# Optimization experiments

Measured on AMD Instinct MI355X. Metric: run time of the kernel, lower is better.

## Reference

```python
import jax, jax.numpy as jnp
import numpy as np

HEADS = 8
DIM_HEAD = 64
INNER = HEADS * DIM_HEAD  # 512
EPS = 1e-6


def layer_norm(x, gamma, beta):
    mu = jnp.mean(x, axis=-1, keepdims=True)
    var = jnp.var(x, axis=-1, keepdims=True)
    return (x - mu) * jax.lax.rsqrt(var + EPS) * gamma + beta


def setup_inputs() -> dict:
    key = jax.random.key(0)
    ks = jax.random.split(key, 8)
    b, n = 2, 2048
    s = lambda d: 1.0 / np.sqrt(d)
    return {
        "x": jax.random.normal(ks[0], (b, n, INNER), dtype=jnp.float32),
        # weights stored input-major: y = x @ W
        "w_qkv": jax.random.normal(ks[1], (INNER, 3 * INNER), dtype=jnp.float32) * s(INNER),
        "w_out": jax.random.normal(ks[2], (INNER, INNER), dtype=jnp.float32) * s(INNER),
        "b_out": jax.random.normal(ks[3], (INNER,), dtype=jnp.float32) * 0.01,
        "w_ff1": jax.random.normal(ks[4], (INNER, 4 * INNER), dtype=jnp.float32) * s(INNER),
        "w_ff2": jax.random.normal(ks[5], (4 * INNER, INNER), dtype=jnp.float32) * s(4 * INNER),
        "g1": jnp.ones((INNER,), dtype=jnp.float32),
        "be1": jnp.zeros((INNER,), dtype=jnp.float32),
        "g2": jnp.ones((INNER,), dtype=jnp.float32),
        "be2": jnp.zeros((INNER,), dtype=jnp.float32),
    }


def reference(x, w_qkv, w_out, b_out, w_ff1, w_ff2, g1, be1, g2, be2):
    b, n, _ = x.shape
    scale = DIM_HEAD ** (-0.5)
    qkv = x @ w_qkv  # [b, n, 3*inner]
    qkv = qkv.reshape(b, n, 3, HEADS, DIM_HEAD)
    q = qkv[:, :, 0].transpose(0, 2, 1, 3)  # [b, h, n, d]
    k = qkv[:, :, 1].transpose(0, 2, 1, 3)
    v = qkv[:, :, 2].transpose(0, 2, 1, 3)
    dots = jnp.einsum('bhqd,bhkd->bhqk', q, k) * scale
    attn = jax.nn.softmax(dots, axis=-1)
    out = jnp.einsum('bhqk,bhkd->bhqd', attn, v)
    out = out.transpose(0, 2, 1, 3).reshape(b, n, INNER)
    out = out @ w_out + b_out
    attn_res = layer_norm(x + out, g1, be1)
    # NOTE: no activation between the two FFN linears (faithful to source)
    ff = (attn_res @ w_ff1) @ w_ff2
    return layer_norm(attn_res + ff, g2, be2)
```

## Files before the change

kernel.cpp:

```cpp
#include <hip/hip_runtime.h>
#include <hip/hip_bf16.h>
#include <cstdint>
#include <cstddef>
#include <math.h>

#define HEADS 8
#define DHEAD 64
#define INNER 512
#define BATCH 2
#define SEQ   2048
#define MROWS (BATCH*SEQ)
#define LN_EPS 1e-6f
#define KSPLIT 4
#define KCHUNK (SEQ/KSPLIT)
#define QSCALE 0.18033688011110918f

typedef unsigned short u16;
typedef __attribute__((ext_vector_type(8))) short short8;
typedef __attribute__((ext_vector_type(4))) short short4v;
typedef __attribute__((ext_vector_type(4))) float f32x4;

#define MFMA16(a,b,c) __builtin_amdgcn_mfma_f32_16x16x32_bf16((a),(b),(c),0,0,0)
#if __has_builtin(__builtin_amdgcn_mfma_f32_16x16x16bf16_1k)
#define HAVE_MFMA16K16 1
#define MFMA16K16(a,b,c) __builtin_amdgcn_mfma_f32_16x16x16bf16_1k((a),(b),(c),0,0,0)
#endif

__device__ __forceinline__ float bf2f(u16 u) {
    union { float f; uint32_t i; } x; x.i = ((uint32_t)u) << 16; return x.f;
}
__device__ __forceinline__ u16 f2bf(float f) {
    __hip_bfloat16 h = __float2bfloat16(f);
    return *reinterpret_cast<u16*>(&h);
}
__device__ __forceinline__ void gl_lds16(const void* g, void* l) {
    __builtin_amdgcn_global_load_lds(
        (const __attribute__((address_space(1))) void*)g,
        (__attribute__((address_space(3))) void*)l, 16, 0, 0);
}

__global__ void prep_kernel(const float* __restrict__ x, u16* __restrict__ x_b,
                            const float* __restrict__ w_qkv, u16* __restrict__ w_qkvT,
                            const float* __restrict__ w_out, u16* __restrict__ w_outT,
                            const float* __restrict__ w_ff1, u16* __restrict__ w_ff1T,
                            const float* __restrict__ w_ff2, u16* __restrict__ w_ff2T) {
    __shared__ float T[32][33];
    const int blk = blockIdx.x, tid = threadIdx.x;
    if (blk < 2048) {
        int i = blk * 256 + tid;
        float4 v = reinterpret_cast<const float4*>(x)[i];
        ushort4 o;
        o.x = f2bf(v.x); o.y = f2bf(v.y); o.z = f2bf(v.z); o.w = f2bf(v.w);
        reinterpret_cast<ushort4*>(x_b)[i] = o;
        return;
    }
    const float* B; u16* Bt; int K, N, t;
    if (blk < 2816)      { B = w_qkv; Bt = w_qkvT; K = 512;  N = 1536; t = blk - 2048; }
    else if (blk < 3072) { B = w_out; Bt = w_outT; K = 512;  N = 512;  t = blk - 2816; }
    else if (blk < 4096) { B = w_ff1; Bt = w_ff1T; K = 512;  N = 2048; t = blk - 3072; }
    else                 { B = w_ff2; Bt = w_ff2T; K = 2048; N = 512;  t = blk - 4096; }
    const int nb = N / 32;
    const int n0 = (t % nb) * 32, k0 = (t / nb) * 32;
    const int r = tid >> 3, c = (tid & 7) * 4;
    float4 v = *reinterpret_cast<const float4*>(&B[(size_t)(k0 + r) * N + n0 + c]);
    T[c + 0][r] = v.x; T[c + 1][r] = v.y; T[c + 2][r] = v.z; T[c + 3][r] = v.w;
    __syncthreads();
    ushort4 o;
    o.x = f2bf(T[r][c + 0]); o.y = f2bf(T[r][c + 1]);
    o.z = f2bf(T[r][c + 2]); o.w = f2bf(T[r][c + 3]);
    *reinterpret_cast<ushort4*>(&Bt[(size_t)(n0 + r) * K + k0 + c]) = o;
}

template<int BN, int EPI>
__global__ __launch_bounds__(256) void gemm_bt(const u16* __restrict__ A,
                                               const u16* __restrict__ Bt,
                                               const float* __restrict__ bias,
                                               float* __restrict__ C,
                                               u16* __restrict__ Cb,
                                               u16* __restrict__ Vt,
                                               int M, int N, int K) {
    constexpr int WN = BN / 2;
    constexpr int NT = WN / 16;
    __shared__ u16 As[128 * 32];
    __shared__ u16 Bs[BN * 32];
    const int tid = threadIdx.x;
    const int wave = tid >> 6, lane = tid & 63;
    const int l15 = lane & 15, quad = lane >> 4;
    const int wm = (wave >> 1) * 64, wn = (wave & 1) * WN;
    const int row0 = blockIdx.y * 128, col0 = blockIdx.x * BN;

    int kbase = 0, kend = K;
    if (EPI == 3) {
        int chunk = K / gridDim.z;
        kbase = blockIdx.z * chunk; kend = kbase + chunk;
    }

    f32x4 acc[4][NT];
    #pragma unroll
    for (int mi = 0; mi < 4; ++mi)
        #pragma unroll
        for (int ni = 0; ni < NT; ++ni)
            #pragma unroll
            for (int e = 0; e < 4; ++e) acc[mi][ni][e] = 0.f;

    for (int k0 = kbase; k0 < kend; k0 += 32) {
        #pragma unroll
        for (int idx0 = 0; idx0 < 512 + BN * 4; idx0 += 256) {
            int idx = idx0 + tid;
            if (idx < 512) {
                int r = idx >> 2, ic = (idx & 3) * 8;
                gl_lds16(A + (size_t)(row0 + r) * K + k0 + ic, &As[idx * 8]);
            } else {
                int ib = idx - 512;
                int r = ib >> 2, ic = (ib & 3) * 8;
                gl_lds16(Bt + (size_t)(col0 + r) * K + k0 + ic, &Bs[ib * 8]);
            }
        }
        __syncthreads();

        short8 af[4], bfr[NT];
        #pragma unroll
        for (int mi = 0; mi < 4; ++mi)
            af[mi] = *reinterpret_cast<const short8*>(&As[(wm + mi * 16 + l15) * 32 + quad * 8]);
        #pragma unroll
        for (int ni = 0; ni < NT; ++ni)
            bfr[ni] = *reinterpret_cast<const short8*>(&Bs[(wn + ni * 16 + l15) * 32 + quad * 8]);
        #pragma unroll
        for (int mi = 0; mi < 4; ++mi)
            #pragma unroll
            for (int ni = 0; ni < NT; ++ni)
                acc[mi][ni] = MFMA16(af[mi], bfr[ni], acc[mi][ni]);
        __syncthreads();
    }

    #pragma unroll
    for (int mi = 0; mi < 4; ++mi)
        #pragma unroll
        for (int ni = 0; ni < NT; ++ni) {
            const int cc = col0 + wn + ni * 16 + l15;
            const int rr0 = row0 + wm + mi * 16 + quad * 4;
            if (EPI == 0) {
                #pragma unroll
                for (int r = 0; r < 4; ++r)
                    Cb[(size_t)(rr0 + r) * N + cc] = f2bf(acc[mi][ni][r]);
            } else if (EPI == 1) {
                #pragma unroll
                for (int r = 0; r < 4; ++r)
                    C[(size_t)(rr0 + r) * N + cc] = acc[mi][ni][r] + bias[cc];
            } else if (EPI == 3) {
                u16* Cz = Cb + (size_t)blockIdx.z * M * N;
                #pragma unroll
                for (int r = 0; r < 4; ++r)
                    Cz[(size_t)(rr0 + r) * N + cc] = f2bf(acc[mi][ni][r]);
            } else {
                if (cc < 1024) {
                    const bool isq = (cc < 512);
                    size_t base = isq ? (size_t)cc
                                      : ((size_t)MROWS * 512 + cc - 512);
                    const float sc = isq ? QSCALE : 1.f;
                    #pragma unroll
                    for (int r = 0; r < 4; ++r)
                        Cb[base + (size_t)(rr0 + r) * 512] = f2bf(acc[mi][ni][r] * sc);
                } else {
                    int hh = (cc - 1024) >> 6, dd = (cc - 1024) & 63;
                    int bb = rr0 >> 11, srow = rr0 & 2047;
                    ushort4 o;
                    o.x = f2bf(acc[mi][ni][0]); o.y = f2bf(acc[mi][ni][1]);
                    o.z = f2bf(acc[mi][ni][2]); o.w = f2bf(acc[mi][ni][3]);
                    *reinterpret_cast<ushort4*>(
                        &Vt[(((size_t)(bb * 8 + hh) * 64 + dd) << 11) + srow]) = o;
                }
            }
        }
}

__global__ __launch_bounds__(256) void attn_kernel(const u16* __restrict__ qk_b,
                                                   const u16* __restrict__ vT_b,
                                                   u16* __restrict__ OpartB,
                                                   float* __restrict__ lpart) {
    __shared__ u16 SM[64 * 64 + 2 * 64 * 72];
    u16 (*Qs)[64] = (u16(*)[64])SM;
    u16 (*Ks)[72] = (u16(*)[72])(SM + 64 * 64);
    u16 (*VT)[72] = (u16(*)[72])(SM + 64 * 64 + 64 * 72);

    const int tid = threadIdx.x;
    const int wave = tid >> 6, lane = tid & 63;
    const int l15 = lane & 15, quad = lane >> 4;
    const int qt = blockIdx.x, bh = blockIdx.y, ks = blockIdx.z;
    const int b = bh >> 3, h = bh & 7;
    const int w16 = wave * 16;
    const int r0 = tid >> 3, r1 = r0 + 32;
    const int ch = (tid & 7) * 8;

    {
        const u16* qb = qk_b + (size_t)(b * SEQ + qt * 64) * 512 + h * 64;
        *reinterpret_cast<uint4*>(&Qs[r0][ch]) =
            *reinterpret_cast<const uint4*>(&qb[(size_t)r0 * 512 + ch]);
        *reinterpret_cast<uint4*>(&Qs[r1][ch]) =
            *reinterpret_cast<const uint4*>(&qb[(size_t)r1 * 512 + ch]);
    }
    __syncthreads();

    short8 qf[2];
    qf[0] = *reinterpret_cast<const short8*>(&Qs[w16 + l15][quad * 8]);
    qf[1] = *reinterpret_cast<const short8*>(&Qs[w16 + l15][32 + quad * 8]);

    const u16* kb = qk_b + (size_t)MROWS * 512
                  + (size_t)(b * SEQ + ks * KCHUNK) * 512 + h * 64;
    const u16* vb = vT_b + (size_t)bh * 64 * 2048 + ks * KCHUNK;

    uint4 kr0 = *reinterpret_cast<const uint4*>(&kb[(size_t)r0 * 512 + ch]);
    uint4 kr1 = *reinterpret_cast<const uint4*>(&kb[(size_t)r1 * 512 + ch]);
    uint4 vr0 = *reinterpret_cast<const uint4*>(&vb[(size_t)r0 * 2048 + ch]);
    uint4 vr1 = *reinterpret_cast<const uint4*>(&vb[(size_t)r1 * 2048 + ch]);

#ifdef HAVE_MFMA16K16
    f32x4 oacc[4];
    float lsum = 0.f;
    #pragma unroll
    for (int di = 0; di < 4; ++di)
        #pragma unroll
        for (int e = 0; e < 4; ++e) oacc[di][e] = 0.f;

    for (int kt = 0; kt < KCHUNK / 64; ++kt) {
        *reinterpret_cast<uint4*>(&Ks[r0][ch]) = kr0;
        *reinterpret_cast<uint4*>(&Ks[r1][ch]) = kr1;
        *reinterpret_cast<uint4*>(&VT[r0][ch]) = vr0;
        *reinterpret_cast<uint4*>(&VT[r1][ch]) = vr1;
        __syncthreads();

        if (kt + 1 < KCHUNK / 64) {
            const u16* kb2 = kb + (size_t)(kt + 1) * 64 * 512;
            const u16* vb2 = vb + (kt + 1) * 64;
            kr0 = *reinterpret_cast<const uint4*>(&kb2[(size_t)r0 * 512 + ch]);
            kr1 = *reinterpret_cast<const uint4*>(&kb2[(size_t)r1 * 512 + ch]);
            vr0 = *reinterpret_cast<const uint4*>(&vb2[(size_t)r0 * 2048 + ch]);
            vr1 = *reinterpret_cast<const uint4*>(&vb2[(size_t)r1 * 2048 + ch]);
        }

        f32x4 sacc[4];
        #pragma unroll
        for (int ni = 0; ni < 4; ++ni)
            #pragma unroll
            for (int e = 0; e < 4; ++e) sacc[ni][e] = 0.f;
        #pragma unroll
        for (int ksk = 0; ksk < 2; ++ksk) {
            short8 kf[4];
            #pragma unroll
            for (int ni = 0; ni < 4; ++ni)
                kf[ni] = *reinterpret_cast<const short8*>(
                    &Ks[ni * 16 + l15][ksk * 32 + quad * 8]);
            #pragma unroll
            for (int ni = 0; ni < 4; ++ni)
                sacc[ni] = MFMA16(kf[ni], qf[ksk], sacc[ni]);
        }

        #pragma unroll
        for (int ni = 0; ni < 4; ++ni) {
            float p0 = exp2f(sacc[ni][0]);
            float p1 = exp2f(sacc[ni][1]);
            float p2 = exp2f(sacc[ni][2]);
            float p3 = exp2f(sacc[ni][3]);
            lsum += (p0 + p1) + (p2 + p3);
            union { short4v v; uint32_t u[2]; } P;
            P.u[0] = __builtin_amdgcn_perm(__float_as_uint(p1),
                                           __float_as_uint(p0), 0x07060302u);
            P.u[1] = __builtin_amdgcn_perm(__float_as_uint(p3),
                                           __float_as_uint(p2), 0x07060302u);
            #pragma unroll
            for (int di = 0; di < 4; ++di) {
                short4v vf = *reinterpret_cast<const short4v*>(
                    &VT[di * 16 + l15][ni * 16 + quad * 4]);
                oacc[di] = MFMA16K16(vf, P.v, oacc[di]);
            }
        }
        __syncthreads();
    }

    lsum += __shfl_xor(lsum, 16);
    lsum += __shfl_xor(lsum, 32);

    const size_t pbase = ((size_t)(ks * 16 + bh) * SEQ + qt * 64);
    if (lane < 16) lpart[pbase + w16 + lane] = lsum;

    float* OTf = (float*)SM;
    #pragma unroll
    for (int di = 0; di < 4; ++di)
        #pragma unroll
        for (int r = 0; r < 4; ++r)
            OTf[(di * 16 + quad * 4 + r) * 68 + w16 + l15] = oacc[di][r];
    __syncthreads();

    const int ql = tid >> 2, dseg = (tid & 3) * 16;
    u16 ov[16];
    #pragma unroll
    for (int i = 0; i < 16; ++i) ov[i] = f2bf(OTf[(dseg + i) * 68 + ql]);
    u16* op = &OpartB[(pbase + ql) * 64 + dseg];
    *reinterpret_cast<uint4*>(op)     = *reinterpret_cast<const uint4*>(ov);
    *reinterpret_cast<uint4*>(op + 8) = *reinterpret_cast<const uint4*>(ov + 8);
#else
    f32x4 oacc[4];
    float lsum[4];
    #pragma unroll
    for (int di = 0; di < 4; ++di)
        #pragma unroll
        for (int e = 0; e < 4; ++e) oacc[di][e] = 0.f;
    #pragma unroll
    for (int r = 0; r < 4; ++r) lsum[r] = 0.f;

    for (int kt = 0; kt < KCHUNK / 64; ++kt) {
        *reinterpret_cast<uint4*>(&Ks[r0][ch]) = kr0;
        *reinterpret_cast<uint4*>(&Ks[r1][ch]) = kr1;
        *reinterpret_cast<uint4*>(&VT[r0][ch]) = vr0;
        *reinterpret_cast<uint4*>(&VT[r1][ch]) = vr1;
        __syncthreads();

        if (kt + 1 < KCHUNK / 64) {
            const u16* kb2 = kb + (size_t)(kt + 1) * 64 * 512;
            const u16* vb2 = vb + (kt + 1) * 64;
            kr0 = *reinterpret_cast<const uint4*>(&kb2[(size_t)r0 * 512 + ch]);
            kr1 = *reinterpret_cast<const uint4*>(&kb2[(size_t)r1 * 512 + ch]);
            vr0 = *reinterpret_cast<const uint4*>(&vb2[(size_t)r0 * 2048 + ch]);
            vr1 = *reinterpret_cast<const uint4*>(&vb2[(size_t)r1 * 2048 + ch]);
        }

        f32x4 sacc[4];
        #pragma unroll
        for (int ni = 0; ni < 4; ++ni)
            #pragma unroll
            for (int e = 0; e < 4; ++e) sacc[ni][e] = 0.f;
        #pragma unroll
        for (int ksk = 0; ksk < 2; ++ksk) {
            short8 kf[4];
            #pragma unroll
            for (int ni = 0; ni < 4; ++ni)
                kf[ni] = *reinterpret_cast<const short8*>(
                    &Ks[ni * 16 + l15][ksk * 32 + quad * 8]);
            #pragma unroll
            for (int ni = 0; ni < 4; ++ni)
                sacc[ni] = MFMA16(qf[ksk], kf[ni], sacc[ni]);
        }
        #pragma unroll
        for (int ni = 0; ni < 4; ++ni)
            #pragma unroll
            for (int r = 0; r < 4; ++r) {
                float p = exp2f(sacc[ni][r]);
                lsum[r] += p;
                Qs[w16 + quad * 4 + r][ni * 16 + l15] = f2bf(p);
            }
        #pragma unroll
        for (int ksk = 0; ksk < 2; ++ksk) {
            short8 pf = *reinterpret_cast<const short8*>(
                &Qs[w16 + l15][ksk * 32 + quad * 8]);
            #pragma unroll
            for (int di = 0; di < 4; ++di) {
                short8 vf = *reinterpret_cast<const short8*>(
                    &VT[di * 16 + l15][ksk * 32 + quad * 8]);
                oacc[di] = MFMA16(pf, vf, oacc[di]);
            }
        }
        __syncthreads();
    }

    #pragma unroll
    for (int r = 0; r < 4; ++r) {
        float v = lsum[r];
        v += __shfl_xor(v, 1); v += __shfl_xor(v, 2);
        v += __shfl_xor(v, 4); v += __shfl_xor(v, 8);
        lsum[r] = v;
    }
    const size_t pbase = ((size_t)(ks * 16 + bh) * SEQ + qt * 64);
    #pragma unroll
    for (int di = 0; di < 4; ++di)
        #pragma unroll
        for (int r = 0; r < 4; ++r)
            OpartB[(pbase + w16 + quad * 4 + r) * 64 + di * 16 + l15] = f2bf(oacc[di][r]);
    if (l15 == 0)
        #pragma unroll
        for (int r = 0; r < 4; ++r)
            lpart[pbase + w16 + quad * 4 + r] = lsum[r];
#endif
}

__global__ void attn_combine_kernel(const u16* __restrict__ OpartB,
                                    const float* __restrict__ lpart,
                                    u16* __restrict__ attn_b) {
    int i = blockIdx.x * 256 + threadIdx.x;
    int e = i * 4;
    int row = e >> 9;
    int c = e & 511;
    int h = c >> 6, d = c & 63;
    int b = row >> 11, srow = row & 2047;
    int bh = b * 8 + h;

    float ax = 0.f, ay = 0.f, az = 0.f, aw = 0.f, l = 0.f;
    #pragma unroll
    for (int ks = 0; ks < KSPLIT; ++ks) {
        size_t pk = (size_t)(ks * 16 + bh) * SEQ + srow;
        ushort4 o = *reinterpret_cast<const ushort4*>(&OpartB[pk * 64 + d]);
        ax += bf2f(o.x); ay += bf2f(o.y); az += bf2f(o.z); aw += bf2f(o.w);
        l += lpart[pk];
    }
    float li = 1.f / l;
    ushort4 o;
    o.x = f2bf(ax * li); o.y = f2bf(ay * li);
    o.z = f2bf(az * li); o.w = f2bf(aw * li);
    *reinterpret_cast<ushort4*>(&attn_b[(size_t)row * INNER + c]) = o;
}

template<bool A16, bool S16, bool TWO>
__global__ __launch_bounds__(256) void ln_kernel(const void* __restrict__ a_,
                                                 const void* __restrict__ s0_,
                                                 const void* __restrict__ s1_,
                                                 const float* __restrict__ g,
                                                 const float* __restrict__ be,
                                                 float* __restrict__ out32,
                                                 u16* __restrict__ out16) {
    const int tid = threadIdx.x, wave = tid >> 6, lane = tid & 63;
    const int row = blockIdx.x * 4 + wave;
    const size_t off = (size_t)row * INNER;

    float v[8];
    #pragma unroll
    for (int j = 0; j < 2; ++j) {
        const int c = j * 256 + lane * 4;
        float a0, a1, a2, a3;
        if (A16) {
            ushort4 u = *reinterpret_cast<const ushort4*>((const u16*)a_ + off + c);
            a0 = bf2f(u.x); a1 = bf2f(u.y); a2 = bf2f(u.z); a3 = bf2f(u.w);
        } else {
            float4 u = *reinterpret_cast<const float4*>((const float*)a_ + off + c);
            a0 = u.x; a1 = u.y; a2 = u.z; a3 = u.w;
        }
        float s0, s1, s2, s3;
        if (S16) {
            ushort4 u = *reinterpret_cast<const ushort4*>((const u16*)s0_ + off + c);
            s0 = bf2f(u.x); s1 = bf2f(u.y); s2 = bf2f(u.z); s3 = bf2f(u.w);
        } else {
            float4 u = *reinterpret_cast<const float4*>((const float*)s0_ + off + c);
            s0 = u.x; s1 = u.y; s2 = u.z; s3 = u.w;
        }
        v[j*4+0] = a0 + s0; v[j*4+1] = a1 + s1; v[j*4+2] = a2 + s2; v[j*4+3] = a3 + s3;
        if (TWO) {
            if (S16) {
                ushort4 u = *reinterpret_cast<const ushort4*>((const u16*)s1_ + off + c);
                v[j*4+0] += bf2f(u.x); v[j*4+1] += bf2f(u.y);
                v[j*4+2] += bf2f(u.z); v[j*4+3] += bf2f(u.w);
            } else {
                float4 u = *reinterpret_cast<const float4*>((const float*)s1_ + off + c);
                v[j*4+0] += u.x; v[j*4+1] += u.y; v[j*4+2] += u.z; v[j*4+3] += u.w;
            }
        }
    }

    float s = 0.f;
    #pragma unroll
    for (int i = 0; i < 8; ++i) s += v[i];
    #pragma unroll
    for (int m = 1; m < 64; m <<= 1) s += __shfl_xor(s, m);
    const float mu = s * (1.f / INNER);

    float q = 0.f;
    #pragma unroll
    for (int i = 0; i < 8; ++i) { v[i] -= mu; q += v[i] * v[i]; }
    #pragma unroll
    for (int m = 1; m < 64; m <<= 1) q += __shfl_xor(q, m);
    const float rstd = rsqrtf(q * (1.f / INNER) + LN_EPS);

    #pragma unroll
    for (int j = 0; j < 2; ++j) {
        const int c = j * 256 + lane * 4;
        float4 gv = *reinterpret_cast<const float4*>(g + c);
        float4 bv = *reinterpret_cast<const float4*>(be + c);
        float y0 = v[j*4+0] * rstd * gv.x + bv.x;
        float y1 = v[j*4+1] * rstd * gv.y + bv.y;
        float y2 = v[j*4+2] * rstd * gv.z + bv.z;
        float y3 = v[j*4+3] * rstd * gv.w + bv.w;
        if (out32) {
            float4 o = {y0, y1, y2, y3};
            *reinterpret_cast<float4*>(out32 + off + c) = o;
        }
        if (out16) {
            ushort4 o;
            o.x = f2bf(y0); o.y = f2bf(y1); o.z = f2bf(y2); o.w = f2bf(y3);
            *reinterpret_cast<ushort4*>(out16 + off + c) = o;
        }
    }
}

extern "C" void kernel_launch(void* const* d_in, const int* in_sizes, int n_in,
                              void* d_out, int out_size, void* d_ws, size_t ws_size,
                              hipStream_t stream) {
    const float* x     = (const float*)d_in[0];
    const float* w_qkv = (const float*)d_in[1];
    const float* w_out = (const float*)d_in[2];
    const float* b_out = (const float*)d_in[3];
    const float* w_ff1 = (const float*)d_in[4];
    const float* w_ff2 = (const float*)d_in[5];
    const float* g1    = (const float*)d_in[6];
    const float* be1   = (const float*)d_in[7];
    const float* g2    = (const float*)d_in[8];
    const float* be2   = (const float*)d_in[9];
    float* out = (float*)d_out;

    char* W = (char*)d_ws;
    u16*   w_outT     = (u16*)  (W + 0);
    u16*   w_ff1T     = (u16*)  (W + 524288);
    u16*   w_ff2T     = (u16*)  (W + 2621440);
    u16*   qk_b       = (u16*)  (W + 4718592);
    float* proj       = (float*)(W + 4718592);
    u16*   ff2p       = (u16*)  (W + 4718592);
    u16*   vT_b       = (u16*)  (W + 13107200);
    u16*   attn_res_b = (u16*)  (W + 13107200);
    u16*   x_b        = (u16*)  (W + 17301504);
    u16*   w_qkvT     = (u16*)  (W + 21495808);
    u16*   OpartB     = (u16*)  (W + 17301504);
    u16*   ff1_b      = (u16*)  (W + 17301504);
    float* lpart      = (float*)(W + 34078720);
    u16*   attn_b     = (u16*)  (W + 34603008);

    prep_kernel<<<5120, 256, 0, stream>>>(x, x_b, w_qkv, w_qkvT, w_out, w_outT,
                                          w_ff1, w_ff1T, w_ff2, w_ff2T);

    gemm_bt<64, 2><<<dim3(1536 / 64, MROWS / 128), 256, 0, stream>>>(
        x_b, w_qkvT, nullptr, nullptr, qk_b, vT_b, MROWS, 1536, INNER);

    attn_kernel<<<dim3(SEQ / 64, BATCH * HEADS, KSPLIT), 256, 0, stream>>>(
        qk_b, vT_b, OpartB, lpart);

    attn_combine_kernel<<<(MROWS * INNER / 4) / 256, 256, 0, stream>>>(
        OpartB, lpart, attn_b);

    gemm_bt<64, 1><<<dim3(INNER / 64, MROWS / 128), 256, 0, stream>>>(
        attn_b, w_outT, b_out, proj, nullptr, nullptr, MROWS, INNER, INNER);

    ln_kernel<false, false, false><<<MROWS / 4, 256, 0, stream>>>(
        x, proj, nullptr, g1, be1, nullptr, attn_res_b);

    gemm_bt<128, 0><<<dim3(2048 / 128, MROWS / 128), 256, 0, stream>>>(
        attn_res_b, w_ff1T, nullptr, nullptr, ff1_b, nullptr, MROWS, 2048, INNER);

    gemm_bt<64, 3><<<dim3(INNER / 64, MROWS / 128, 2), 256, 0, stream>>>(
        ff1_b, w_ff2T, nullptr, nullptr, ff2p, nullptr, MROWS, INNER, 2048);

    ln_kernel<true, true, true><<<MROWS / 4, 256, 0, stream>>>(
        attn_res_b, ff2p, ff2p + (size_t)MROWS * INNER, g2, be2, out, nullptr);
}
```

Before: 211.0 us.

## Process two query tiles per attention block and deepen GEMM K-tile to 64

The attention kernel now handles 128 query rows per block as two 64-row sub-tiles, reusing each staged K/V tile and its register fragments for both. This halves K/V global and LDS traffic per query and halves the attention grid. Separately, the GEMM template gains a BK parameter set to 64, halving the number of barrier-separated k-iterations at the cost of double the LDS per block. Both raise register and LDS pressure, which may lower occupancy, and the smaller attention grid may underfill the GPU.

```diff
diff --git a/kernel.cpp b/kernel.cpp
--- a/kernel.cpp
+++ b/kernel.cpp
@@ -71,7 +71,7 @@
     *reinterpret_cast<ushort4*>(&Bt[(size_t)(n0 + r) * K + k0 + c]) = o;
 }
 
-template<int BN, int EPI>
+template<int BN, int BK, int EPI>
 __global__ __launch_bounds__(256) void gemm_bt(const u16* __restrict__ A,
                                                const u16* __restrict__ Bt,
                                                const float* __restrict__ bias,
@@ -81,8 +81,11 @@
                                                int M, int N, int K) {
     constexpr int WN = BN / 2;
     constexpr int NT = WN / 16;
-    __shared__ u16 As[128 * 32];
-    __shared__ u16 Bs[BN * 32];
+    constexpr int ACH = 128 * BK / 8;
+    constexpr int BCH = BN * BK / 8;
+    constexpr int CW = BK / 8;
+    __shared__ u16 As[128 * BK];
+    __shared__ u16 Bs[BN * BK];
     const int tid = threadIdx.x;
     const int wave = tid >> 6, lane = tid & 63;
     const int l15 = lane & 15, quad = lane >> 4;
@@ -103,33 +106,38 @@
             #pragma unroll
             for (int e = 0; e < 4; ++e) acc[mi][ni][e] = 0.f;
 
-    for (int k0 = kbase; k0 < kend; k0 += 32) {
-        #pragma unroll
-        for (int idx0 = 0; idx0 < 512 + BN * 4; idx0 += 256) {
+    for (int k0 = kbase; k0 < kend; k0 += BK) {
+        #pragma unroll
+        for (int idx0 = 0; idx0 < ACH + BCH; idx0 += 256) {
             int idx = idx0 + tid;
-            if (idx < 512) {
-                int r = idx >> 2, ic = (idx & 3) * 8;
+            if (idx < ACH) {
+                int r = idx / CW, ic = (idx % CW) * 8;
                 gl_lds16(A + (size_t)(row0 + r) * K + k0 + ic, &As[idx * 8]);
             } else {
-                int ib = idx - 512;
-                int r = ib >> 2, ic = (ib & 3) * 8;
+                int ib = idx - ACH;
+                int r = ib / CW, ic = (ib % CW) * 8;
                 gl_lds16(Bt + (size_t)(col0 + r) * K + k0 + ic, &Bs[ib * 8]);
             }
         }
         __syncthreads();
 
-        short8 af[4], bfr[NT];
-        #pragma unroll
-        for (int mi = 0; mi < 4; ++mi)
-            af[mi] = *reinterpret_cast<const short8*>(&As[(wm + mi * 16 + l15) * 32 + quad * 8]);
-        #pragma unroll
-        for (int ni = 0; ni < NT; ++ni)
-            bfr[ni] = *reinterpret_cast<const short8*>(&Bs[(wn + ni * 16 + l15) * 32 + quad * 8]);
-        #pragma unroll
-        for (int mi = 0; mi < 4; ++mi)
+        #pragma unroll
+        for (int ks2 = 0; ks2 < BK / 32; ++ks2) {
+            short8 af[4], bfr[NT];
+            #pragma unroll
+            for (int mi = 0; mi < 4; ++mi)
+                af[mi] = *reinterpret_cast<const short8*>(
+                    &As[(wm + mi * 16 + l15) * BK + ks2 * 32 + quad * 8]);
             #pragma unroll
             for (int ni = 0; ni < NT; ++ni)
-                acc[mi][ni] = MFMA16(af[mi], bfr[ni], acc[mi][ni]);
+                bfr[ni] = *reinterpret_cast<const short8*>(
+                    &Bs[(wn + ni * 16 + l15) * BK + ks2 * 32 + quad * 8]);
+            #pragma unroll
+            for (int mi = 0; mi < 4; ++mi)
+                #pragma unroll
+                for (int ni = 0; ni < NT; ++ni)
+                    acc[mi][ni] = MFMA16(af[mi], bfr[ni], acc[mi][ni]);
+        }
         __syncthreads();
     }
 
@@ -178,10 +186,10 @@
                                                    const u16* __restrict__ vT_b,
                                                    u16* __restrict__ OpartB,
                                                    float* __restrict__ lpart) {
-    __shared__ u16 SM[64 * 64 + 2 * 64 * 72];
+    __shared__ u16 SM[2 * 64 * 64 + 2 * 64 * 72];
     u16 (*Qs)[64] = (u16(*)[64])SM;
-    u16 (*Ks)[72] = (u16(*)[72])(SM + 64 * 64);
-    u16 (*VT)[72] = (u16(*)[72])(SM + 64 * 64 + 64 * 72);
+    u16 (*Ks)[72] = (u16(*)[72])(SM + 2 * 64 * 64);
+    u16 (*VT)[72] = (u16(*)[72])(SM + 2 * 64 * 64 + 64 * 72);
 
     const int tid = threadIdx.x;
     const int wave = tid >> 6, lane = tid & 63;
@@ -193,17 +201,23 @@
     const int ch = (tid & 7) * 8;
 
     {
-        const u16* qb = qk_b + (size_t)(b * SEQ + qt * 64) * 512 + h * 64;
-        *reinterpret_cast<uint4*>(&Qs[r0][ch]) =
-            *reinterpret_cast<const uint4*>(&qb[(size_t)r0 * 512 + ch]);
-        *reinterpret_cast<uint4*>(&Qs[r1][ch]) =
-            *reinterpret_cast<const uint4*>(&qb[(size_t)r1 * 512 + ch]);
+        const u16* qb = qk_b + (size_t)(b * SEQ + qt * 128) * 512 + h * 64;
+        #pragma unroll
+        for (int j = 0; j < 4; ++j) {
+            int idx = tid + j * 256;
+            int r = idx >> 3, c = (idx & 7) * 8;
+            *reinterpret_cast<uint4*>(&Qs[r][c]) =
+                *reinterpret_cast<const uint4*>(&qb[(size_t)r * 512 + c]);
+        }
     }
     __syncthreads();
 
-    short8 qf[2];
-    qf[0] = *reinterpret_cast<const short8*>(&Qs[w16 + l15][quad * 8]);
-    qf[1] = *reinterpret_cast<const short8*>(&Qs[w16 + l15][32 + quad * 8]);
+    short8 qf[2][2];
+    #pragma unroll
+    for (int t = 0; t < 2; ++t) {
+        qf[t][0] = *reinterpret_cast<const short8*>(&Qs[t * 64 + w16 + l15][quad * 8]);
+        qf[t][1] = *reinterpret_cast<const short8*>(&Qs[t * 64 + w16 + l15][32 + quad * 8]);
+    }
 
     const u16* kb = qk_b + (size_t)MROWS * 512
                   + (size_t)(b * SEQ + ks * KCHUNK) * 512 + h * 64;
@@ -215,12 +229,14 @@
     uint4 vr1 = *reinterpret_cast<const uint4*>(&vb[(size_t)r1 * 2048 + ch]);
 
 #ifdef HAVE_MFMA16K16
-    f32x4 oacc[4];
-    float lsum = 0.f;
-    #pragma unroll
-    for (int di = 0; di < 4; ++di)
-        #pragma unroll
-        for (int e = 0; e < 4; ++e) oacc[di][e] = 0.f;
+    f32x4 oacc[2][4];
+    float lsum[2] = {0.f, 0.f};
+    #pragma unroll
+    for (int t = 0; t < 2; ++t)
+        #pragma unroll
+        for (int di = 0; di < 4; ++di)
+            #pragma unroll
+            for (int e = 0; e < 4; ++e) oacc[t][di][e] = 0.f;
 
     for (int kt = 0; kt < KCHUNK / 64; ++kt) {
         *reinterpret_cast<uint4*>(&Ks[r0][ch]) = kr0;
@@ -238,75 +254,93 @@
             vr1 = *reinterpret_cast<const uint4*>(&vb2[(size_t)r1 * 2048 + ch]);
         }
 
-        f32x4 sacc[4];
+        short8 kf[4];
         #pragma unroll
         for (int ni = 0; ni < 4; ++ni)
-            #pragma unroll
-            for (int e = 0; e < 4; ++e) sacc[ni][e] = 0.f;
-        #pragma unroll
-        for (int ksk = 0; ksk < 2; ++ksk) {
-            short8 kf[4];
+            kf[ni] = *reinterpret_cast<const short8*>(&Ks[ni * 16 + l15][quad * 8]);
+        short8 kf2[4];
+        #pragma unroll
+        for (int ni = 0; ni < 4; ++ni)
+            kf2[ni] = *reinterpret_cast<const short8*>(&Ks[ni * 16 + l15][32 + quad * 8]);
+
+        #pragma unroll
+        for (int t = 0; t < 2; ++t) {
+            f32x4 sacc[4];
             #pragma unroll
             for (int ni = 0; ni < 4; ++ni)
-                kf[ni] = *reinterpret_cast<const short8*>(
-                    &Ks[ni * 16 + l15][ksk * 32 + quad * 8]);
+                #pragma unroll
+                for (int e = 0; e < 4; ++e) sacc[ni][e] = 0.f;
             #pragma unroll
             for (int ni = 0; ni < 4; ++ni)
-                sacc[ni] = MFMA16(kf[ni], qf[ksk], sacc[ni]);
-        }
-
-        #pragma unroll
-        for (int ni = 0; ni < 4; ++ni) {
-            float p0 = exp2f(sacc[ni][0]);
-            float p1 = exp2f(sacc[ni][1]);
-            float p2 = exp2f(sacc[ni][2]);
-            float p3 = exp2f(sacc[ni][3]);
-            lsum += (p0 + p1) + (p2 + p3);
-            union { short4v v; uint32_t u[2]; } P;
-            P.u[0] = __builtin_amdgcn_perm(__float_as_uint(p1),
-                                           __float_as_uint(p0), 0x07060302u);
-            P.u[1] = __builtin_amdgcn_perm(__float_as_uint(p3),
-                                           __float_as_uint(p2), 0x07060302u);
-            #pragma unroll
-            for (int di = 0; di < 4; ++di) {
-                short4v vf = *reinterpret_cast<const short4v*>(
-                    &VT[di * 16 + l15][ni * 16 + quad * 4]);
-                oacc[di] = MFMA16K16(vf, P.v, oacc[di]);
+                sacc[ni] = MFMA16(kf[ni], qf[t][0], sacc[ni]);
+            #pragma unroll
+            for (int ni = 0; ni < 4; ++ni)
+                sacc[ni] = MFMA16(kf2[ni], qf[t][1], sacc[ni]);
+
+            #pragma unroll
+            for (int ni = 0; ni < 4; ++ni) {
+                float p0 = exp2f(sacc[ni][0]);
+                float p1 = exp2f(sacc[ni][1]);
+                float p2 = exp2f(sacc[ni][2]);
+                float p3 = exp2f(sacc[ni][3]);
+                lsum[t] += (p0 + p1) + (p2 + p3);
+                union { short4v v; uint32_t u[2]; } P;
+                P.u[0] = __builtin_amdgcn_perm(__float_as_uint(p1),
+                                               __float_as_uint(p0), 0x07060302u);
+                P.u[1] = __builtin_amdgcn_perm(__float_as_uint(p3),
+                                               __float_as_uint(p2), 0x07060302u);
+                #pragma unroll
+                for (int di = 0; di < 4; ++di) {
+                    short4v vf = *reinterpret_cast<const short4v*>(
+                        &VT[di * 16 + l15][ni * 16 + quad * 4]);
+                    oacc[t][di] = MFMA16K16(vf, P.v, oacc[t][di]);
+                }
             }
         }
         __syncthreads();
     }
 
-    lsum += __shfl_xor(lsum, 16);
-    lsum += __shfl_xor(lsum, 32);
-
-    const size_t pbase = ((size_t)(ks * 16 + bh) * SEQ + qt * 64);
-    if (lane < 16) lpart[pbase + w16 + lane] = lsum;
+    #pragma unroll
+    for (int t = 0; t < 2; ++t) {
+        lsum[t] += __shfl_xor(lsum[t], 16);
+        lsum[t] += __shfl_xor(lsum[t], 32);
+    }
+
+    const size_t pbase = ((size_t)(ks * 16 + bh) * SEQ + qt * 128);
+    if (lane < 16) {
+        lpart[pbase + w16 + lane] = lsum[0];
+        lpart[pbase + 64 + w16 + lane] = lsum[1];
+    }
 
     float* OTf = (float*)SM;
-    #pragma unroll
-    for (int di = 0; di < 4; ++di)
-        #pragma unroll
-        for (int r = 0; r < 4; ++r)
-            OTf[(di * 16 + quad * 4 + r) * 68 + w16 + l15] = oacc[di][r];
-    __syncthreads();
-
     const int ql = tid >> 2, dseg = (tid & 3) * 16;
-    u16 ov[16];
-    #pragma unroll
-    for (int i = 0; i < 16; ++i) ov[i] = f2bf(OTf[(dseg + i) * 68 + ql]);
-    u16* op = &OpartB[(pbase + ql) * 64 + dseg];
-    *reinterpret_cast<uint4*>(op)     = *reinterpret_cast<const uint4*>(ov);
-    *reinterpret_cast<uint4*>(op + 8) = *reinterpret_cast<const uint4*>(ov + 8);
+    #pragma unroll
+    for (int t = 0; t < 2; ++t) {
+        __syncthreads();
+        #pragma unroll
+        for (int di = 0; di < 4; ++di)
+            #pragma unroll
+            for (int r = 0; r < 4; ++r)
+                OTf[(di * 16 + quad * 4 + r) * 68 + w16 + l15] = oacc[t][di][r];
+        __syncthreads();
+        u16 ov[16];
+        #pragma unroll
+        for (int i = 0; i < 16; ++i) ov[i] = f2bf(OTf[(dseg + i) * 68 + ql]);
+        u16* op = &OpartB[(pbase + t * 64 + ql) * 64 + dseg];
+        *reinterpret_cast<uint4*>(op)     = *reinterpret_cast<const uint4*>(ov);
+        *reinterpret_cast<uint4*>(op + 8) = *reinterpret_cast<const uint4*>(ov + 8);
+    }
 #else
-    f32x4 oacc[4];
-    float lsum[4];
-    #pragma unroll
-    for (int di = 0; di < 4; ++di)
-        #pragma unroll
-        for (int e = 0; e < 4; ++e) oacc[di][e] = 0.f;
-    #pragma unroll
-    for (int r = 0; r < 4; ++r) lsum[r] = 0.f;
+    f32x4 oacc[2][4];
+    float lsum[2][4];
+    #pragma unroll
+    for (int t = 0; t < 2; ++t)
+        #pragma unroll
+        for (int di = 0; di < 4; ++di) {
+            #pragma unroll
+            for (int e = 0; e < 4; ++e) oacc[t][di][e] = 0.f;
+            lsum[t][di] = 0.f;
+        }
 
     for (int kt = 0; kt < KCHUNK / 64; ++kt) {
         *reinterpret_cast<uint4*>(&Ks[r0][ch]) = kr0;
@@ -324,61 +358,68 @@
             vr1 = *reinterpret_cast<const uint4*>(&vb2[(size_t)r1 * 2048 + ch]);
         }
 
-        f32x4 sacc[4];
-        #pragma unroll
-        for (int ni = 0; ni < 4; ++ni)
-            #pragma unroll
-            for (int e = 0; e < 4; ++e) sacc[ni][e] = 0.f;
-        #pragma unroll
-        for (int ksk = 0; ksk < 2; ++ksk) {
-            short8 kf[4];
+        #pragma unroll
+        for (int t = 0; t < 2; ++t) {
+            f32x4 sacc[4];
             #pragma unroll
             for (int ni = 0; ni < 4; ++ni)
-                kf[ni] = *reinterpret_cast<const short8*>(
-                    &Ks[ni * 16 + l15][ksk * 32 + quad * 8]);
+                #pragma unroll
+                for (int e = 0; e < 4; ++e) sacc[ni][e] = 0.f;
+            #pragma unroll
+            for (int ksk = 0; ksk < 2; ++ksk) {
+                short8 kf[4];
+                #pragma unroll
+                for (int ni = 0; ni < 4; ++ni)
+                    kf[ni] = *reinterpret_cast<const short8*>(
+                        &Ks[ni * 16 + l15][ksk * 32 + quad * 8]);
+                #pragma unroll
+                for (int ni = 0; ni < 4; ++ni)
+                    sacc[ni] = MFMA16(qf[t][ksk], kf[ni], sacc[ni]);
+            }
             #pragma unroll
             for (int ni = 0; ni < 4; ++ni)
-                sacc[ni] = MFMA16(qf[ksk], kf[ni], sacc[ni]);
-        }
-        #pragma unroll
-        for (int ni = 0; ni < 4; ++ni)
-            #pragma unroll
-            for (int r = 0; r < 4; ++r) {
-                float p = exp2f(sacc[ni][r]);
-                lsum[r] += p;
-                Qs[w16 + quad * 4 + r][ni * 16 + l15] = f2bf(p);
+                #pragma unroll
+                for (int r = 0; r < 4; ++r) {
+                    float p = exp2f(sacc[ni][r]);
+                    lsum[t][r] += p;
+                    Qs[t * 64 + w16 + quad * 4 + r][ni * 16 + l15] = f2bf(p);
+                }
+            #pragma unroll
+            for (int ksk = 0; ksk < 2; ++ksk) {
+                short8 pf = *reinterpret_cast<const short8*>(
+                    &Qs[t * 64 + w16 + l15][ksk * 32 + quad * 8]);
+                #pragma unroll
+                for (int di = 0; di < 4; ++di) {
+                    short8 vf = *reinterpret_cast<const short8*>(
+                        &VT[di * 16 + l15][ksk * 32 + quad * 8]);
+                    oacc[t][di] = MFMA16(pf, vf, oacc[t][di]);
+                }
             }
-        #pragma unroll
-        for (int ksk = 0; ksk < 2; ++ksk) {
-            short8 pf = *reinterpret_cast<const short8*>(
-                &Qs[w16 + l15][ksk * 32 + quad * 8]);
-            #pragma unroll
-            for (int di = 0; di < 4; ++di) {
-                short8 vf = *reinterpret_cast<const short8*>(
-                    &VT[di * 16 + l15][ksk * 32 + quad * 8]);
-                oacc[di] = MFMA16(pf, vf, oacc[di]);
-            }
-        }
-        __syncthreads();
-    }
-
-    #pragma unroll
-    for (int r = 0; r < 4; ++r) {
-        float v = lsum[r];
-        v += __shfl_xor(v, 1); v += __shfl_xor(v, 2);
-        v += __shfl_xor(v, 4); v += __shfl_xor(v, 8);
-        lsum[r] = v;
-    }
-    const size_t pbase = ((size_t)(ks * 16 + bh) * SEQ + qt * 64);
-    #pragma unroll
-    for (int di = 0; di < 4; ++di)
-        #pragma unroll
-        for (int r = 0; r < 4; ++r)
-            OpartB[(pbase + w16 + quad * 4 + r) * 64 + di * 16 + l15] = f2bf(oacc[di][r]);
-    if (l15 == 0)
-        #pragma unroll
-        for (int r = 0; r < 4; ++r)
-            lpart[pbase + w16 + quad * 4 + r] = lsum[r];
+        }
+        __syncthreads();
+    }
+
+    const size_t pbase = ((size_t)(ks * 16 + bh) * SEQ + qt * 128);
+    #pragma unroll
+    for (int t = 0; t < 2; ++t) {
+        #pragma unroll
+        for (int r = 0; r < 4; ++r) {
+            float v = lsum[t][r];
+            v += __shfl_xor(v, 1); v += __shfl_xor(v, 2);
+            v += __shfl_xor(v, 4); v += __shfl_xor(v, 8);
+            lsum[t][r] = v;
+        }
+        #pragma unroll
+        for (int di = 0; di < 4; ++di)
+            #pragma unroll
+            for (int r = 0; r < 4; ++r)
+                OpartB[(pbase + t * 64 + w16 + quad * 4 + r) * 64 + di * 16 + l15]
+                    = f2bf(oacc[t][di][r]);
+        if (l15 == 0)
+            #pragma unroll
+            for (int r = 0; r < 4; ++r)
+                lpart[pbase + t * 64 + w16 + quad * 4 + r] = lsum[t][r];
+    }
 #endif
 }
 
@@ -522,25 +563,25 @@
     prep_kernel<<<5120, 256, 0, stream>>>(x, x_b, w_qkv, w_qkvT, w_out, w_outT,
                                           w_ff1, w_ff1T, w_ff2, w_ff2T);
 
-    gemm_bt<64, 2><<<dim3(1536 / 64, MROWS / 128), 256, 0, stream>>>(
+    gemm_bt<64, 64, 2><<<dim3(1536 / 64, MROWS / 128), 256, 0, stream>>>(
         x_b, w_qkvT, nullptr, nullptr, qk_b, vT_b, MROWS, 1536, INNER);
 
-    attn_kernel<<<dim3(SEQ / 64, BATCH * HEADS, KSPLIT), 256, 0, stream>>>(
+    attn_kernel<<<dim3(SEQ / 128, BATCH * HEADS, KSPLIT), 256, 0, stream>>>(
         qk_b, vT_b, OpartB, lpart);
 
     attn_combine_kernel<<<(MROWS * INNER / 4) / 256, 256, 0, stream>>>(
         OpartB, lpart, attn_b);
 
-    gemm_bt<64, 1><<<dim3(INNER / 64, MROWS / 128), 256, 0, stream>>>(
+    gemm_bt<64, 64, 1><<<dim3(INNER / 64, MROWS / 128), 256, 0, stream>>>(
         attn_b, w_outT, b_out, proj, nullptr, nullptr, MROWS, INNER, INNER);
 
     ln_kernel<false, false, false><<<MROWS / 4, 256, 0, stream>>>(
         x, proj, nullptr, g1, be1, nullptr, attn_res_b);
 
-    gemm_bt<128, 0><<<dim3(2048 / 128, MROWS / 128), 256, 0, stream>>>(
+    gemm_bt<128, 64, 0><<<dim3(2048 / 128, MROWS / 128), 256, 0, stream>>>(
         attn_res_b, w_ff1T, nullptr, nullptr, ff1_b, nullptr, MROWS, 2048, INNER);
 
-    gemm_bt<64, 3><<<dim3(INNER / 64, MROWS / 128, 2), 256, 0, stream>>>(
+    gemm_bt<64, 64, 3><<<dim3(INNER / 64, MROWS / 128, 2), 256, 0, stream>>>(
         ff1_b, w_ff2T, nullptr, nullptr, ff2p, nullptr, MROWS, INNER, 2048);
 
     ln_kernel<true, true, true><<<MROWS / 4, 256, 0, stream>>>(
```

New measurement: 206.8 us. 1.02x faster.
